# Kernel tuning notes

Measured on AMD Instinct MI355X. Metric: run time of the kernel, lower is better.

The kernel has to match this reference:

```python
import jax, jax.numpy as jnp
import numpy as np

B = 131072
IN_DIM = 100
H = 256


def setup_inputs() -> dict:
    key = jax.random.key(0)
    ks = jax.random.split(key, 7)
    return {
        "x": jax.random.normal(ks[0], (B, IN_DIM), dtype=jnp.float32),
        "C": jax.random.normal(ks[1], (B, H), dtype=jnp.float32),
        "h": jax.random.normal(ks[2], (B, H), dtype=jnp.float32),
        # stacked gate weights, gate order: i, f, g, o  (equivalent to 8 separate Linears)
        "Wx": jax.random.normal(ks[3], (IN_DIM, 4 * H), dtype=jnp.float32) * 0.05,
        "Wh": jax.random.normal(ks[4], (H, 4 * H), dtype=jnp.float32) * 0.05,
        "bx": jax.random.normal(ks[5], (4 * H,), dtype=jnp.float32) * 0.05,
        "bh": jax.random.normal(ks[6], (4 * H,), dtype=jnp.float32) * 0.05,
    }


def reference(x, C, h, Wx, Wh, bx, bh):
    # two fused GEMMs replace the 8 per-gate Linears (same math)
    gates = (x @ Wx + bx) + (h @ Wh + bh)  # [B, 4H]
    i_pre, f_pre, g_pre, o_pre = jnp.split(gates, 4, axis=-1)
    i = jax.nn.sigmoid(i_pre)
    f = jax.nn.sigmoid(f_pre)
    g = jnp.tanh(g_pre)
    o = jax.nn.sigmoid(o_pre)
    c_out = f * C + i * g
    h_out = o * jnp.tanh(c_out)
    return (c_out, h_out)
```

## Files before the change

### kernel.cpp

```cpp
#include <hip/hip_runtime.h>
#include <stdint.h>


typedef short          bf16x8 __attribute__((ext_vector_type(8)));
typedef unsigned short u16x8  __attribute__((ext_vector_type(8)));
typedef float          f32x4  __attribute__((ext_vector_type(4)));

#define HDIM   256
#define INDIM  100
#define NROWS  131072
#define NSTAGE 6

__device__ __forceinline__ float fexp(float x) {
  return __builtin_amdgcn_exp2f(x * 1.44269504088896340736f);
}
__device__ __forceinline__ float frcp(float x) { return __builtin_amdgcn_rcpf(x); }
__device__ __forceinline__ float sigm(float x) { return frcp(1.0f + fexp(-x)); }
__device__ __forceinline__ float tanh_fast(float x) {
  return 1.0f - 2.0f * frcp(1.0f + fexp(2.0f * x));
}
__device__ __forceinline__ unsigned short f2bf_rne(float f) {
  union { float f; uint32_t u; } v; v.f = f;
  return (unsigned short)((v.u + 0x7FFFu + ((v.u >> 16) & 1u)) >> 16);
}
__device__ __forceinline__ unsigned int cvt_pk_bf16(float lo, float hi) {
  unsigned int r;
  asm("v_cvt_pk_bf16_f32 %0, %1, %2" : "=v"(r) : "v"(lo), "v"(hi));
  return r;
}

__global__ void prep_w(const float* __restrict__ Wx, const float* __restrict__ Wh,
                       unsigned short* __restrict__ Bt) {
  const int unit = blockIdx.x * 4 + (threadIdx.x >> 6);
  const int lane = threadIdx.x & 63;
  const int kst  = unit % 12;
  const int fidb = unit / 12;
  const int bn   = fidb >> 3, fid = fidb & 7;
  const int g    = fid >> 1,  wc  = fid & 1;
  const int wcol = g * HDIM + bn * 32 + wc * 16 + (lane & 15);
  const int kb   = kst * 32 + (lane >> 4) * 8;
  unsigned short v[8];
#pragma unroll
  for (int e = 0; e < 8; ++e) {
    const int k = kb + e;
    float f = 0.0f;
    if (k < INDIM)       f = Wx[(size_t)k * 1024 + wcol];
    else if (k >= 128)   f = Wh[(size_t)(k - 128) * 1024 + wcol];
    v[e] = f2bf_rne(f);
  }
  *reinterpret_cast<u16x8*>(Bt + (size_t)unit * 512 + lane * 8) =
      *reinterpret_cast<u16x8*>(v);
}

__global__ __launch_bounds__(256, 3)
void lstm_main(const float* __restrict__ X, const float* __restrict__ Cin,
               const float* __restrict__ Hin,
               const unsigned short* __restrict__ Bt,
               const float* __restrict__ bxp, const float* __restrict__ bhp,
               float* __restrict__ out)
{
  __shared__ unsigned short As[2][128 * 64];

  const int tid  = threadIdx.x;
  const int orig = blockIdx.x;
  const int lg   = ((orig & 7) << 10) | (orig >> 3);
  const int mt   = lg >> 3;
  const int bn   = lg & 7;

  const int lane = tid & 63;
  const int l15  = lane & 15;
  const int kq   = lane >> 4;
  const int wid  = tid >> 6;
  const int wr   = wid >> 1;
  const int wc   = wid & 1;

  f32x4 acc[4][4];
#pragma unroll
  for (int m = 0; m < 4; ++m)
#pragma unroll
    for (int g = 0; g < 4; ++g)
#pragma unroll
      for (int e = 0; e < 4; ++e) acc[m][g][e] = 0.0f;

  float av[32];

  auto stage_load = [&](int s) {
    const bool   xph = (s < 2);
    const float* Ap  = xph ? X : Hin;
    const int    lda = xph ? INDIM : HDIM;
    const int    kb  = xph ? s * 64 : (s - 2) * 64;
#pragma unroll
    for (int i = 0; i < 4; ++i) {
      const int ci = i * 256 + tid;
      const int r  = ci >> 3, c = ci & 7;
      const int k0 = kb + c * 8;
      const float* p = Ap + (size_t)(mt * 128 + r) * lda + k0;
      float4 lo = make_float4(0.f, 0.f, 0.f, 0.f);
      float4 hi = make_float4(0.f, 0.f, 0.f, 0.f);
      if (k0 + 4 <= lda) lo = *reinterpret_cast<const float4*>(p);
      if (k0 + 8 <= lda) hi = *reinterpret_cast<const float4*>(p + 4);
      av[i*8+0]=lo.x; av[i*8+1]=lo.y; av[i*8+2]=lo.z; av[i*8+3]=lo.w;
      av[i*8+4]=hi.x; av[i*8+5]=hi.y; av[i*8+6]=hi.z; av[i*8+7]=hi.w;
    }
  };

  auto stage_write = [&](int b) {
#pragma unroll
    for (int i = 0; i < 4; ++i) {
      const int ci = i * 256 + tid;
      const int r  = ci >> 3, c = ci & 7;
      unsigned int u[4];
#pragma unroll
      for (int j = 0; j < 4; ++j)
        u[j] = cvt_pk_bf16(av[i*8 + 2*j], av[i*8 + 2*j + 1]);
      *reinterpret_cast<uint4*>(&As[b][r * 64 + ((c ^ (r & 7)) * 8)]) =
          *reinterpret_cast<uint4*>(u);
    }
  };

  stage_load(0);
  stage_write(0);
  __syncthreads();

#pragma unroll
  for (int s = 0; s < NSTAGE; ++s) {
    if (s + 1 < NSTAGE) stage_load(s + 1);

    bf16x8 bfr[2][4];
#pragma unroll
    for (int kk = 0; kk < 2; ++kk)
#pragma unroll
      for (int g = 0; g < 4; ++g) {
        const int fid = g * 2 + wc;
        const size_t off =
            ((size_t)((bn * 8 + fid) * 12 + (s * 2 + kk))) * 512 + lane * 8;
        bfr[kk][g] = *reinterpret_cast<const bf16x8*>(Bt + off);
      }

    const unsigned short* Ab = As[s & 1];
#pragma unroll
    for (int kk = 0; kk < 2; ++kk) {
      bf16x8 afr[4];
#pragma unroll
      for (int m = 0; m < 4; ++m) {
        const int row = wr * 64 + m * 16 + l15;
        afr[m] = *reinterpret_cast<const bf16x8*>(
            &Ab[row * 64 + (((kk * 4 + kq) ^ (row & 7)) * 8)]);
      }
      __builtin_amdgcn_s_setprio(1);
#pragma unroll
      for (int m = 0; m < 4; ++m)
#pragma unroll
        for (int g = 0; g < 4; ++g)
          acc[m][g] = __builtin_amdgcn_mfma_f32_16x16x32_bf16(
              afr[m], bfr[kk][g], acc[m][g], 0, 0, 0);
      __builtin_amdgcn_s_setprio(0);
    }

    if (s + 1 < NSTAGE) stage_write((s + 1) & 1);
    __syncthreads();
  }

  const int ch = bn * 32 + wc * 16 + l15;
  float bias[4];
#pragma unroll
  for (int g = 0; g < 4; ++g) bias[g] = bxp[g * HDIM + ch] + bhp[g * HDIM + ch];

  const size_t HTOT = (size_t)NROWS * HDIM;
#pragma unroll
  for (int m = 0; m < 4; ++m) {
#pragma unroll
    for (int e = 0; e < 4; ++e) {
      const int r = mt * 128 + wr * 64 + m * 16 + kq * 4 + e;
      const float pi = acc[m][0][e] + bias[0];
      const float pf = acc[m][1][e] + bias[1];
      const float pg = acc[m][2][e] + bias[2];
      const float po = acc[m][3][e] + bias[3];
      const float Cv = Cin[(size_t)r * HDIM + ch];
      const float ig = sigm(pi), fg = sigm(pf);
      const float gg = tanh_fast(pg), og = sigm(po);
      const float co = fg * Cv + ig * gg;
      const float ho = og * tanh_fast(co);
      out[(size_t)r * HDIM + ch]        = co;
      out[HTOT + (size_t)r * HDIM + ch] = ho;
    }
  }
}

extern "C" void kernel_launch(void* const* d_in, const int* in_sizes, int n_in,
                              void* d_out, int out_size, void* d_ws, size_t ws_size,
                              hipStream_t stream) {
  const float* x  = (const float*)d_in[0];
  const float* C  = (const float*)d_in[1];
  const float* h  = (const float*)d_in[2];
  const float* Wx = (const float*)d_in[3];
  const float* Wh = (const float*)d_in[4];
  const float* bx = (const float*)d_in[5];
  const float* bh = (const float*)d_in[6];
  float* o = (float*)d_out;
  unsigned short* Bt = (unsigned short*)d_ws;

  prep_w<<<dim3(192), dim3(256), 0, stream>>>(Wx, Wh, Bt);
  lstm_main<<<dim3(8192), dim3(256), 0, stream>>>(x, C, h, Bt, bx, bh, o);
}
```

Measured before the change: 232.6 us.

## Load A fragments directly from global into registers, dropping LDS staging

Removes the shared-memory double buffer and barriers; each lane now loads its own MFMA A fragment straight from X/H in global memory, converts to bf16 in registers, and runs 12 k-chunks with no syncthreads. The C input values are also prefetched into registers before the epilogue. This removes LDS traffic and barrier stalls, but the global loads are now strided per row (32-byte pieces per lane), two column-tile blocks read the same rows redundantly through cache, and there is no explicit software prefetch overlapping loads with MFMA.

```diff
diff --git a/kernel.cpp b/kernel.cpp
--- a/kernel.cpp
+++ b/kernel.cpp
@@ -5,11 +5,11 @@
 typedef short          bf16x8 __attribute__((ext_vector_type(8)));
 typedef unsigned short u16x8  __attribute__((ext_vector_type(8)));
 typedef float          f32x4  __attribute__((ext_vector_type(4)));
+typedef unsigned int   u32x4  __attribute__((ext_vector_type(4)));
 
 #define HDIM   256
 #define INDIM  100
 #define NROWS  131072
-#define NSTAGE 6
 
 __device__ __forceinline__ float fexp(float x) {
   return __builtin_amdgcn_exp2f(x * 1.44269504088896340736f);
@@ -59,8 +59,6 @@
                const float* __restrict__ bxp, const float* __restrict__ bhp,
                float* __restrict__ out)
 {
-  __shared__ unsigned short As[2][128 * 64];
-
   const int tid  = threadIdx.x;
   const int orig = blockIdx.x;
   const int lg   = ((orig & 7) << 10) | (orig >> 3);
@@ -73,6 +71,20 @@
   const int wid  = tid >> 6;
   const int wr   = wid >> 1;
   const int wc   = wid & 1;
+  const int ch   = bn * 32 + wc * 16 + l15;
+
+  const float* xrp[4];
+  const float* hrp[4];
+#pragma unroll
+  for (int m = 0; m < 4; ++m) {
+    const int row = mt * 128 + wr * 64 + m * 16 + l15;
+    xrp[m] = X   + (size_t)row * INDIM + kq * 8;
+    hrp[m] = Hin + (size_t)row * HDIM + kq * 8;
+  }
+  const unsigned short* btp[4];
+#pragma unroll
+  for (int g = 0; g < 4; ++g)
+    btp[g] = Bt + (size_t)((bn * 8 + g * 2 + wc) * 12) * 512 + lane * 8;
 
   f32x4 acc[4][4];
 #pragma unroll
@@ -82,107 +94,73 @@
 #pragma unroll
       for (int e = 0; e < 4; ++e) acc[m][g][e] = 0.0f;
 
-  float av[32];
+#pragma unroll
+  for (int c = 0; c < 12; ++c) {
+    bf16x8 bfr[4];
+#pragma unroll
+    for (int g = 0; g < 4; ++g)
+      bfr[g] = *reinterpret_cast<const bf16x8*>(btp[g] + c * 512);
 
-  auto stage_load = [&](int s) {
-    const bool   xph = (s < 2);
-    const float* Ap  = xph ? X : Hin;
-    const int    lda = xph ? INDIM : HDIM;
-    const int    kb  = xph ? s * 64 : (s - 2) * 64;
+    bf16x8 afr[4];
 #pragma unroll
-    for (int i = 0; i < 4; ++i) {
-      const int ci = i * 256 + tid;
-      const int r  = ci >> 3, c = ci & 7;
-      const int k0 = kb + c * 8;
-      const float* p = Ap + (size_t)(mt * 128 + r) * lda + k0;
+    for (int m = 0; m < 4; ++m) {
       float4 lo = make_float4(0.f, 0.f, 0.f, 0.f);
       float4 hi = make_float4(0.f, 0.f, 0.f, 0.f);
-      if (k0 + 4 <= lda) lo = *reinterpret_cast<const float4*>(p);
-      if (k0 + 8 <= lda) hi = *reinterpret_cast<const float4*>(p + 4);
-      av[i*8+0]=lo.x; av[i*8+1]=lo.y; av[i*8+2]=lo.z; av[i*8+3]=lo.w;
-      av[i*8+4]=hi.x; av[i*8+5]=hi.y; av[i*8+6]=hi.z; av[i*8+7]=hi.w;
-    }
-  };
-
-  auto stage_write = [&](int b) {
-#pragma unroll
-    for (int i = 0; i < 4; ++i) {
-      const int ci = i * 256 + tid;
-      const int r  = ci >> 3, c = ci & 7;
-      unsigned int u[4];
-#pragma unroll
-      for (int j = 0; j < 4; ++j)
-        u[j] = cvt_pk_bf16(av[i*8 + 2*j], av[i*8 + 2*j + 1]);
-      *reinterpret_cast<uint4*>(&As[b][r * 64 + ((c ^ (r & 7)) * 8)]) =
-          *reinterpret_cast<uint4*>(u);
-    }
-  };
-
-  stage_load(0);
-  stage_write(0);
-  __syncthreads();
-
-#pragma unroll
-  for (int s = 0; s < NSTAGE; ++s) {
-    if (s + 1 < NSTAGE) stage_load(s + 1);
-
-    bf16x8 bfr[2][4];
-#pragma unroll
-    for (int kk = 0; kk < 2; ++kk)
-#pragma unroll
-      for (int g = 0; g < 4; ++g) {
-        const int fid = g * 2 + wc;
-        const size_t off =
-            ((size_t)((bn * 8 + fid) * 12 + (s * 2 + kk))) * 512 + lane * 8;
-        bfr[kk][g] = *reinterpret_cast<const bf16x8*>(Bt + off);
+      if (c < 3) {
+        lo = *reinterpret_cast<const float4*>(xrp[m] + c * 32);
+        hi = *reinterpret_cast<const float4*>(xrp[m] + c * 32 + 4);
+      } else if (c == 3) {
+        if (kq == 0) lo = *reinterpret_cast<const float4*>(xrp[m] + 96);
+      } else {
+        lo = *reinterpret_cast<const float4*>(hrp[m] + (c - 4) * 32);
+        hi = *reinterpret_cast<const float4*>(hrp[m] + (c - 4) * 32 + 4);
       }
-
-    const unsigned short* Ab = As[s & 1];
-#pragma unroll
-    for (int kk = 0; kk < 2; ++kk) {
-      bf16x8 afr[4];
-#pragma unroll
-      for (int m = 0; m < 4; ++m) {
-        const int row = wr * 64 + m * 16 + l15;
-        afr[m] = *reinterpret_cast<const bf16x8*>(
-            &Ab[row * 64 + (((kk * 4 + kq) ^ (row & 7)) * 8)]);
-      }
-      __builtin_amdgcn_s_setprio(1);
-#pragma unroll
-      for (int m = 0; m < 4; ++m)
-#pragma unroll
-        for (int g = 0; g < 4; ++g)
-          acc[m][g] = __builtin_amdgcn_mfma_f32_16x16x32_bf16(
-              afr[m], bfr[kk][g], acc[m][g], 0, 0, 0);
-      __builtin_amdgcn_s_setprio(0);
+      union { u32x4 u; bf16x8 b; } cv;
+      cv.u[0] = cvt_pk_bf16(lo.x, lo.y);
+      cv.u[1] = cvt_pk_bf16(lo.z, lo.w);
+      cv.u[2] = cvt_pk_bf16(hi.x, hi.y);
+      cv.u[3] = cvt_pk_bf16(hi.z, hi.w);
+      afr[m] = cv.b;
     }
 
-    if (s + 1 < NSTAGE) stage_write((s + 1) & 1);
-    __syncthreads();
+    __builtin_amdgcn_s_setprio(1);
+#pragma unroll
+    for (int m = 0; m < 4; ++m)
+#pragma unroll
+      for (int g = 0; g < 4; ++g)
+        acc[m][g] = __builtin_amdgcn_mfma_f32_16x16x32_bf16(
+            afr[m], bfr[g], acc[m][g], 0, 0, 0);
+    __builtin_amdgcn_s_setprio(0);
   }
 
-  const int ch = bn * 32 + wc * 16 + l15;
   float bias[4];
 #pragma unroll
   for (int g = 0; g < 4; ++g) bias[g] = bxp[g * HDIM + ch] + bhp[g * HDIM + ch];
 
-  const size_t HTOT = (size_t)NROWS * HDIM;
+  float cvv[4][4];
+  const float* cbase = Cin + (size_t)(mt * 128 + wr * 64 + kq * 4) * HDIM + ch;
+#pragma unroll
+  for (int m = 0; m < 4; ++m)
+#pragma unroll
+    for (int e = 0; e < 4; ++e)
+      cvv[m][e] = cbase[(size_t)(m * 16 + e) * HDIM];
+
+  float* obase = out + (size_t)(mt * 128 + wr * 64 + kq * 4) * HDIM + ch;
+  float* obase2 = obase + (size_t)NROWS * HDIM;
 #pragma unroll
   for (int m = 0; m < 4; ++m) {
 #pragma unroll
     for (int e = 0; e < 4; ++e) {
-      const int r = mt * 128 + wr * 64 + m * 16 + kq * 4 + e;
       const float pi = acc[m][0][e] + bias[0];
       const float pf = acc[m][1][e] + bias[1];
       const float pg = acc[m][2][e] + bias[2];
       const float po = acc[m][3][e] + bias[3];
-      const float Cv = Cin[(size_t)r * HDIM + ch];
       const float ig = sigm(pi), fg = sigm(pf);
       const float gg = tanh_fast(pg), og = sigm(po);
-      const float co = fg * Cv + ig * gg;
+      const float co = fg * cvv[m][e] + ig * gg;
       const float ho = og * tanh_fast(co);
-      out[(size_t)r * HDIM + ch]        = co;
-      out[HTOT + (size_t)r * HDIM + ch] = ho;
+      obase [(size_t)(m * 16 + e) * HDIM] = co;
+      obase2[(size_t)(m * 16 + e) * HDIM] = ho;
     }
   }
 }
```

Result: slower. 405.5 us (+74.3%).

## Deepen global-load prefetch to two stages and prefetch C/bias early

Applied to the files above, without the earlier changes.

Activation tiles are now loaded two stages ahead into alternating register buffers, so each global load has a full extra MFMA stage to complete. The C-state values and biases are fetched during stage 4 instead of after the GEMM, hiding their latency behind compute. The full __syncthreads is replaced by an lgkmcnt-only wait plus s_barrier, and launch bounds drop from 3 to 2 blocks per SIMD to make room for the extra 32+16 registers. The cost is lower occupancy, which may reduce latency hiding across blocks.

```diff
diff --git a/kernel.cpp b/kernel.cpp
--- a/kernel.cpp
+++ b/kernel.cpp
@@ -10,6 +10,8 @@
 #define INDIM  100
 #define NROWS  131072
 #define NSTAGE 6
+
+#define BAR() asm volatile("s_waitcnt lgkmcnt(0)\n\ts_barrier" ::: "memory")
 
 __device__ __forceinline__ float fexp(float x) {
   return __builtin_amdgcn_exp2f(x * 1.44269504088896340736f);
@@ -52,7 +54,7 @@
       *reinterpret_cast<u16x8*>(v);
 }
 
-__global__ __launch_bounds__(256, 3)
+__global__ __launch_bounds__(256, 2)
 void lstm_main(const float* __restrict__ X, const float* __restrict__ Cin,
                const float* __restrict__ Hin,
                const unsigned short* __restrict__ Bt,
@@ -73,6 +75,7 @@
   const int wid  = tid >> 6;
   const int wr   = wid >> 1;
   const int wc   = wid & 1;
+  const int ch   = bn * 32 + wc * 16 + l15;
 
   f32x4 acc[4][4];
 #pragma unroll
@@ -82,9 +85,9 @@
 #pragma unroll
       for (int e = 0; e < 4; ++e) acc[m][g][e] = 0.0f;
 
-  float av[32];
-
-  auto stage_load = [&](int s) {
+  float avA[32], avB[32];
+
+  auto stage_load = [&](int s, float (&av)[32]) {
     const bool   xph = (s < 2);
     const float* Ap  = xph ? X : Hin;
     const int    lda = xph ? INDIM : HDIM;
@@ -104,7 +107,7 @@
     }
   };
 
-  auto stage_write = [&](int b) {
+  auto stage_write = [&](int b, float (&av)[32]) {
 #pragma unroll
     for (int i = 0; i < 4; ++i) {
       const int ci = i * 256 + tid;
@@ -118,24 +121,41 @@
     }
   };
 
-  stage_load(0);
-  stage_write(0);
-  __syncthreads();
+  stage_load(0, avA);
+  stage_load(1, avB);
+  stage_write(0, avA);
+  BAR();
+
+  float cvv[16];
+  float bias[4];
+  const float* cbase = Cin + (size_t)(mt * 128 + wr * 64 + kq * 4) * HDIM + ch;
 
 #pragma unroll
   for (int s = 0; s < NSTAGE; ++s) {
-    if (s + 1 < NSTAGE) stage_load(s + 1);
-
     bf16x8 bfr[2][4];
 #pragma unroll
     for (int kk = 0; kk < 2; ++kk)
 #pragma unroll
       for (int g = 0; g < 4; ++g) {
-        const int fid = g * 2 + wc;
         const size_t off =
-            ((size_t)((bn * 8 + fid) * 12 + (s * 2 + kk))) * 512 + lane * 8;
+            ((size_t)((bn * 8 + g * 2 + wc) * 12 + (s * 2 + kk))) * 512 + lane * 8;
         bfr[kk][g] = *reinterpret_cast<const bf16x8*>(Bt + off);
       }
+
+    if (s + 2 < NSTAGE) {
+      if ((s & 1) == 0) stage_load(s + 2, avA);
+      else              stage_load(s + 2, avB);
+    }
+    if (s == 4) {
+#pragma unroll
+      for (int m = 0; m < 4; ++m)
+#pragma unroll
+        for (int e = 0; e < 4; ++e)
+          cvv[m * 4 + e] = cbase[(size_t)(m * 16 + e) * HDIM];
+#pragma unroll
+      for (int g = 0; g < 4; ++g)
+        bias[g] = bxp[g * HDIM + ch] + bhp[g * HDIM + ch];
+    }
 
     const unsigned short* Ab = As[s & 1];
 #pragma unroll
@@ -157,32 +177,29 @@
       __builtin_amdgcn_s_setprio(0);
     }
 
-    if (s + 1 < NSTAGE) stage_write((s + 1) & 1);
-    __syncthreads();
+    if (s + 1 < NSTAGE) {
+      if ((s & 1) == 0) stage_write((s + 1) & 1, avB);
+      else              stage_write((s + 1) & 1, avA);
+      BAR();
+    }
   }
 
-  const int ch = bn * 32 + wc * 16 + l15;
-  float bias[4];
-#pragma unroll
-  for (int g = 0; g < 4; ++g) bias[g] = bxp[g * HDIM + ch] + bhp[g * HDIM + ch];
-
-  const size_t HTOT = (size_t)NROWS * HDIM;
+  float* obase  = out + (size_t)(mt * 128 + wr * 64 + kq * 4) * HDIM + ch;
+  float* obase2 = obase + (size_t)NROWS * HDIM;
 #pragma unroll
   for (int m = 0; m < 4; ++m) {
 #pragma unroll
     for (int e = 0; e < 4; ++e) {
-      const int r = mt * 128 + wr * 64 + m * 16 + kq * 4 + e;
       const float pi = acc[m][0][e] + bias[0];
       const float pf = acc[m][1][e] + bias[1];
       const float pg = acc[m][2][e] + bias[2];
       const float po = acc[m][3][e] + bias[3];
-      const float Cv = Cin[(size_t)r * HDIM + ch];
       const float ig = sigm(pi), fg = sigm(pf);
       const float gg = tanh_fast(pg), og = sigm(po);
-      const float co = fg * Cv + ig * gg;
+      const float co = fg * cvv[m * 4 + e] + ig * gg;
       const float ho = og * tanh_fast(co);
-      out[(size_t)r * HDIM + ch]        = co;
-      out[HTOT + (size_t)r * HDIM + ch] = ho;
+      obase [(size_t)(m * 16 + e) * HDIM] = co;
+      obase2[(size_t)(m * 16 + e) * HDIM] = ho;
     }
   }
 }
```

After: 236.4 us. No clear change (+1.6%).
